# Kernel tuning notes

Measured on AMD Instinct MI355X. Metric: run time of the kernel, lower is better.

The kernel has to match this reference:

```python
import jax, jax.numpy as jnp
import numpy as np

SCALE = 2
K = 5          # up_kernel
GROUPS = 1     # up_group
COMP = 64      # compressed_channels


def _conv2d(x, w, b, padding):
    out = jax.lax.conv_general_dilated(
        x, w, window_strides=(1, 1),
        padding=[(padding, padding), (padding, padding)],
        dimension_numbers=('NCHW', 'OIHW', 'NCHW'))
    return out + b[None, :, None, None]


def _pixel_shuffle(x, r):
    b, crr, h, w = x.shape
    c = crr // (r * r)
    x = x.reshape(b, c, r, r, h, w)
    x = x.transpose(0, 1, 4, 2, 5, 3)  # b, c, h, r, w, r
    return x.reshape(b, c, h * r, w * r)


def setup_inputs() -> dict:
    key = jax.random.key(0)
    k1, k2, k3 = jax.random.split(key, 3)
    C = 256
    x = jax.random.normal(k1, (4, C, 128, 128), dtype=jnp.float32)
    mask_ch = SCALE * SCALE * K * K * GROUPS  # 100
    W1 = jax.random.normal(k2, (COMP, C, 1, 1), dtype=jnp.float32) * 0.05
    b1 = jnp.zeros((COMP,), dtype=jnp.float32)
    W2 = jax.random.normal(k3, (mask_ch, COMP, 3, 3), dtype=jnp.float32) * 0.05
    b2 = jnp.zeros((mask_ch,), dtype=jnp.float32)
    return {'x': x, 'W1': W1, 'b1': b1, 'W2': W2, 'b2': b2}


def reference(x, W1, b1, W2, b2):
    b, c, h, w = x.shape
    s, k, g = SCALE, K, GROUPS
    H, W = h * s, w * s
    # channel compressor (1x1) + mask encoder (3x3, pad 1)
    feat = _conv2d(x, W1, b1, 0)
    mask = _conv2d(feat, W2, b2, 1)            # (b, s^2*k^2*g, h, w)
    mask = _pixel_shuffle(mask, s)             # (b, k^2*g, H, W)
    mask = mask.reshape(b, g, k * k, H, W)
    mask = jax.nn.softmax(mask, axis=2)
    # nearest upsample
    x_up = jnp.repeat(jnp.repeat(x, s, axis=2), s, axis=3)  # (b, c, H, W)
    pad = k // 2
    xp = jnp.pad(x_up, ((0, 0), (0, 0), (pad, pad), (pad, pad)))
    xg = xp.reshape(b, g, c // g, H + 2 * pad, W + 2 * pad)
    # fused gather-multiply-reduce over the k*k window (avoids the huge unfold tensor)
    out = jnp.zeros((b, g, c // g, H, W), x.dtype)
    for i in range(k):
        for j in range(k):
            out = out + xg[:, :, :, i:i + H, j:j + W] * mask[:, :, None, i * k + j]
    return out.reshape(b, c, H, W)
```

## Files before the change

kernel.cpp:

```cpp
#include <hip/hip_runtime.h>

#define HW 16384
#define CIN 256
#define NCOMP 64
#define MASKC 100
#define NB 4
#define COPAD 112
#define KSTEPS 18

typedef __attribute__((ext_vector_type(8))) short bf16x8;
typedef __attribute__((ext_vector_type(4))) float f32x4;
typedef __attribute__((ext_vector_type(4), aligned(4))) float f4u;

__device__ inline ushort f2bf(float f) {
  uint x = __float_as_uint(f);
  return (ushort)((x + 0x7fffu + ((x >> 16) & 1u)) >> 16);
}

__device__ __forceinline__ void softmax_agg(const float* ldsM, int px, int rr,
                                            int h, float* wr9) {
  #pragma unroll
  for (int i = 0; i < 9; i++) wr9[i] = 0.f;

  float m[25], mx = -1e30f;
  #pragma unroll
  for (int kk = 0; kk < 25; kk++) {
    m[kk] = ldsM[(kk * 2 + (rr & 1)) * 129 + px];
    mx = fmaxf(mx, m[kk]);
  }
  float s = 0.f;
  #pragma unroll
  for (int kk = 0; kk < 25; kk++) { m[kk] = __expf(m[kk] - mx); s += m[kk]; }
  float inv = 1.f / s;
  const int r1 = rr >> 1, r2 = rr & 1;
  #pragma unroll
  for (int i = 0; i < 5; i++)
    #pragma unroll
    for (int j = 0; j < 5; j++) {
      const int dy = (r1 + i - 2) >> 1;
      const int dx = (r2 + j - 2) >> 1;
      wr9[(dy + 1) * 3 + (dx + 1)] += m[i * 5 + j] * inv;
    }

  #pragma unroll
  for (int dy = -1; dy <= 1; dy++) {
    bool vy = (unsigned)(h + dy) < 128u;
    #pragma unroll
    for (int dx = -1; dx <= 1; dx++) {
      bool vx = (unsigned)(px + dx) < 128u;
      if (!(vy && vx)) wr9[(dy + 1) * 3 + dx + 1] = 0.f;
    }
  }
}

__global__ __launch_bounds__(512) void conv1x1_mfma(const float* __restrict__ x,
    const ushort* __restrict__ W1b, const float* __restrict__ b1,
    ushort* __restrict__ feat_t) {
  int tid = threadIdx.x, bid = blockIdx.x;
  int b = bid >> 7, h = bid & 127;
  int wave = tid >> 6, lane = tid & 63;
  int l15 = lane & 15, l4 = lane >> 4;

  const float* xb = x + ((size_t)b << 22) + h * 128;
  int n = wave * 16 + l15;

  f32x4 acc[4];
  #pragma unroll
  for (int mt = 0; mt < 4; mt++) acc[mt] = (f32x4){0.f, 0.f, 0.f, 0.f};

  #pragma unroll
  for (int s = 0; s < 8; s++) {
    int k0 = s * 32 + l4 * 8;
    union { bf16x8 v; ushort us[8]; } bf;
    #pragma unroll
    for (int j = 0; j < 8; j++)
      bf.us[j] = f2bf(xb[((size_t)(k0 + j) << 14) + n]);
    #pragma unroll
    for (int mt = 0; mt < 4; mt++) {
      bf16x8 af = *(const bf16x8*)(W1b + (((mt * 8 + s) << 6) + lane) * 8);
      acc[mt] = __builtin_amdgcn_mfma_f32_16x16x32_bf16(af, bf.v, acc[mt], 0, 0, 0);
    }
  }

  ushort* fb = feat_t + (((size_t)(b << 14) + h * 128 + n) << 6);
  #pragma unroll
  for (int mt = 0; mt < 4; mt++) {
    float4 bv = *(const float4*)(b1 + mt * 16 + l4 * 4);
    const float* bvp = (const float*)&bv;
    uint u0 = (uint)f2bf(acc[mt][0] + bvp[0]) | ((uint)f2bf(acc[mt][1] + bvp[1]) << 16);
    uint u1 = (uint)f2bf(acc[mt][2] + bvp[2]) | ((uint)f2bf(acc[mt][3] + bvp[3]) << 16);
    uint2 st; st.x = u0; st.y = u1;
    *(uint2*)(fb + mt * 16 + l4 * 4) = st;
  }
}

__global__ __launch_bounds__(256) void wprep_k(const float* __restrict__ W2,
    const float* __restrict__ W1, ushort* __restrict__ Wr,
    ushort* __restrict__ W1b) {
  int i = blockIdx.x * 256 + threadIdx.x;
  if (i < 64512) {
    int e = i & 7, lane = (i >> 3) & 63, sm = i >> 9;
    int s = sm % 18, mt = sm / 18;
    int l15 = lane & 15, l4 = lane >> 4;
    int co = mt * 16 + l15;
    int ci = (s & 1) * 32 + l4 * 8 + e;
    int k = s >> 1;
    float v = (co < MASKC) ? W2[(co * 64 + ci) * 9 + k] : 0.f;
    Wr[i] = f2bf(v);
  } else if (i < 64512 + 16384) {
    int j = i - 64512;
    int e = j & 7, lane = (j >> 3) & 63, sm = j >> 9;
    int s = sm & 7, mt = sm >> 3;
    int l15 = lane & 15, l4 = lane >> 4;
    int co = mt * 16 + l15;
    int ci = s * 32 + l4 * 8 + e;
    W1b[j] = f2bf(W1[co * 256 + ci]);
  }
}

__global__ __launch_bounds__(512, 4) void conv3x3_combine(const ushort* __restrict__ feat_t,
    const ushort* __restrict__ Wr, const float* __restrict__ b2,
    const float* __restrict__ x, float* __restrict__ out) {
  __shared__ __align__(16) char smem[50 * 129 * 4 + 64];
  int tid = threadIdx.x;
  int wid = (blockIdx.x & 7) * 64 + (blockIdx.x >> 3);
  int b = wid >> 7, h = wid & 127;
  int wave = tid >> 6, lane = tid & 63;
  int l15 = lane & 15, l4 = lane >> 4;

  f32x4 acc[7];
  #pragma unroll
  for (int mt = 0; mt < 7; mt++) acc[mt] = (f32x4){0.f, 0.f, 0.f, 0.f};

  int cb = wave * 16;
  const ushort* fb = feat_t + (((size_t)b << 14) << 6);

  #pragma unroll
  for (int s = 0; s < KSTEPS; s++) {
    const int k = s >> 1;
    const int r = k / 3;
    const int dx = k % 3 - 1;
    const int ci0 = (s & 1) * 32;

    int hh = h - 1 + r;
    int gc = cb + l15 + dx;
    bf16x8 bfrag = {0, 0, 0, 0, 0, 0, 0, 0};
    if ((unsigned)hh < 128u && (unsigned)gc < 128u)
      bfrag = *(const bf16x8*)(fb + (((size_t)(hh * 128 + gc)) << 6) + ci0 + l4 * 8);

    #pragma unroll
    for (int mt = 0; mt < 7; mt++) {
      bf16x8 afrag = *(const bf16x8*)(Wr + (((mt * 18 + s) << 6) + lane) * 8);
      acc[mt] = __builtin_amdgcn_mfma_f32_16x16x32_bf16(afrag, bfrag, acc[mt], 0, 0, 0);
    }
  }

  float* ldsM = (float*)smem;
  float wr9[9];
  int px = tid & 127, rr = tid >> 7;

  #pragma unroll
  for (int mt = 0; mt < 7; mt++) {
    int kkd = mt * 4 + l4;
    if (kkd < 25) {
      int co0 = mt * 16 + l4 * 4;
      ldsM[(kkd * 2 + 0) * 129 + cb + l15] = acc[mt][0] + b2[co0 + 0];
      ldsM[(kkd * 2 + 1) * 129 + cb + l15] = acc[mt][1] + b2[co0 + 1];
    }
  }
  __syncthreads();

  if (rr < 2) softmax_agg(ldsM, px, rr, h, wr9);
  __syncthreads();

  #pragma unroll
  for (int mt = 0; mt < 7; mt++) {
    int kkd = mt * 4 + l4;
    if (kkd < 25) {
      int co0 = mt * 16 + l4 * 4;
      ldsM[(kkd * 2 + 0) * 129 + cb + l15] = acc[mt][2] + b2[co0 + 2];
      ldsM[(kkd * 2 + 1) * 129 + cb + l15] = acc[mt][3] + b2[co0 + 3];
    }
  }
  __syncthreads();

  if (rr >= 2) softmax_agg(ldsM, px, rr, h, wr9);
  __syncthreads();

  float* wlds = (float*)smem;
  {
    #pragma unroll
    for (int i = 0; i < 9; i++) wlds[px * 37 + rr * 9 + i] = wr9[i];
  }
  __syncthreads();

  {
    int pp = tid & 63, g = tid >> 6;
    int w0 = pp * 2;
    float wcA[36], wcB[36];
    #pragma unroll
    for (int i = 0; i < 36; i++) wcA[i] = wlds[w0 * 37 + i];
    #pragma unroll
    for (int i = 0; i < 36; i++) wcB[i] = wlds[(w0 + 1) * 37 + i];

    int cc0 = w0 - 1;
    cc0 = (cc0 < 0) ? 0 : ((cc0 > 124) ? 124 : cc0);
    int off = w0 - 1 - cc0;
    bool o0 = (off == 0), om = (off < 0);

    int ys[3] = {max(h - 1, 0) * 128, h * 128, min(h + 1, 127) * 128};
    const float* xbase = x + ((size_t)b << 22) + cc0;
    float* ob = out + (((size_t)b * CIN) << 16) + ((2 * h) << 8) + 4 * pp;

    #pragma unroll 2
    for (int cc = 0; cc < 32; cc++) {
      int c = cc * 8 + g;
      const float* xc = xbase + ((size_t)c << 14);
      float a0 = 0.f, a1 = 0.f, a2 = 0.f, a3 = 0.f;
      float b0 = 0.f, b1v = 0.f, b2v = 0.f, b3 = 0.f;
      #pragma unroll
      for (int dy = 0; dy < 3; dy++) {
        f4u f = *(const f4u*)(xc + ys[dy]);
        float vA0 = o0 ? f[0] : (om ? 0.f  : f[1]);
        float vA1 = o0 ? f[1] : (om ? f[0] : f[2]);
        float vA2 = o0 ? f[2] : (om ? f[1] : f[3]);
        float vB2 = o0 ? f[3] : (om ? f[2] : 0.f);
        a0 += wcA[0*9+dy*3+0]*vA0 + wcA[0*9+dy*3+1]*vA1 + wcA[0*9+dy*3+2]*vA2;
        a1 += wcA[1*9+dy*3+0]*vA0 + wcA[1*9+dy*3+1]*vA1 + wcA[1*9+dy*3+2]*vA2;
        a2 += wcA[2*9+dy*3+0]*vA0 + wcA[2*9+dy*3+1]*vA1 + wcA[2*9+dy*3+2]*vA2;
        a3 += wcA[3*9+dy*3+0]*vA0 + wcA[3*9+dy*3+1]*vA1 + wcA[3*9+dy*3+2]*vA2;
        b0  += wcB[0*9+dy*3+0]*vA1 + wcB[0*9+dy*3+1]*vA2 + wcB[0*9+dy*3+2]*vB2;
        b1v += wcB[1*9+dy*3+0]*vA1 + wcB[1*9+dy*3+1]*vA2 + wcB[1*9+dy*3+2]*vB2;
        b2v += wcB[2*9+dy*3+0]*vA1 + wcB[2*9+dy*3+1]*vA2 + wcB[2*9+dy*3+2]*vB2;
        b3  += wcB[3*9+dy*3+0]*vA1 + wcB[3*9+dy*3+1]*vA2 + wcB[3*9+dy*3+2]*vB2;
      }
      float* oc = ob + ((size_t)c << 16);
      float4 o0v; o0v.x = a0; o0v.y = a1; o0v.z = b0;  o0v.w = b1v;
      float4 o1v; o1v.x = a2; o1v.y = a3; o1v.z = b2v; o1v.w = b3;
      *(float4*)(oc) = o0v;
      *(float4*)(oc + 256) = o1v;
    }
  }
}

extern "C" void kernel_launch(void* const* d_in, const int* in_sizes, int n_in,
                              void* d_out, int out_size, void* d_ws, size_t ws_size,
                              hipStream_t stream) {
  const float* x  = (const float*)d_in[0];
  const float* W1 = (const float*)d_in[1];
  const float* b1 = (const float*)d_in[2];
  const float* W2 = (const float*)d_in[3];
  const float* b2 = (const float*)d_in[4];
  float* out  = (float*)d_out;

  char* ws = (char*)d_ws;
  ushort* feat_t = (ushort*)ws;
  ushort* Wr     = (ushort*)(ws + 8388608);
  ushort* W1b    = (ushort*)(ws + 8388608 + 129024);

  wprep_k<<<316, 256, 0, stream>>>(W2, W1, Wr, W1b);
  conv1x1_mfma<<<NB * 128, 512, 0, stream>>>(x, W1b, b1, feat_t);
  conv3x3_combine<<<NB * 128, 512, 0, stream>>>(feat_t, Wr, b2, x, out);
}
```

Baseline: 108.1 us.

## Split fused conv3x3+combine into mask kernel and separate wider-grid combine kernel

Splits the fused conv3x3/softmax/combine kernel in two. The first kernel writes the aggregated 3x3 mask weights (36 floats per pixel) to a workspace buffer. A new combine kernel then reads them with a 2D grid that spreads channels over four blocks per row. The goal is more parallelism and occupancy for the bandwidth-bound combine stage, which no longer shares the register and LDS footprint of the MFMA phase. The cost is one extra launch and a global write/read of about 9 MB of weights.

```diff
diff --git a/kernel.cpp b/kernel.cpp
--- a/kernel.cpp
+++ b/kernel.cpp
@@ -118,9 +118,9 @@
   }
 }
 
-__global__ __launch_bounds__(512, 4) void conv3x3_combine(const ushort* __restrict__ feat_t,
+__global__ __launch_bounds__(512, 4) void conv3x3_mask(const ushort* __restrict__ feat_t,
     const ushort* __restrict__ Wr, const float* __restrict__ b2,
-    const float* __restrict__ x, float* __restrict__ out) {
+    float* __restrict__ wagg) {
   __shared__ __align__(16) char smem[50 * 129 * 4 + 64];
   int tid = threadIdx.x;
   int wid = (blockIdx.x & 7) * 64 + (blockIdx.x >> 3);
@@ -195,51 +195,77 @@
   __syncthreads();
 
   {
-    int pp = tid & 63, g = tid >> 6;
-    int w0 = pp * 2;
-    float wcA[36], wcB[36];
-    #pragma unroll
-    for (int i = 0; i < 36; i++) wcA[i] = wlds[w0 * 37 + i];
-    #pragma unroll
-    for (int i = 0; i < 36; i++) wcB[i] = wlds[(w0 + 1) * 37 + i];
-
-    int cc0 = w0 - 1;
-    cc0 = (cc0 < 0) ? 0 : ((cc0 > 124) ? 124 : cc0);
-    int off = w0 - 1 - cc0;
-    bool o0 = (off == 0), om = (off < 0);
-
-    int ys[3] = {max(h - 1, 0) * 128, h * 128, min(h + 1, 127) * 128};
-    const float* xbase = x + ((size_t)b << 22) + cc0;
-    float* ob = out + (((size_t)b * CIN) << 16) + ((2 * h) << 8) + 4 * pp;
-
-    #pragma unroll 2
-    for (int cc = 0; cc < 32; cc++) {
-      int c = cc * 8 + g;
-      const float* xc = xbase + ((size_t)c << 14);
-      float a0 = 0.f, a1 = 0.f, a2 = 0.f, a3 = 0.f;
-      float b0 = 0.f, b1v = 0.f, b2v = 0.f, b3 = 0.f;
-      #pragma unroll
-      for (int dy = 0; dy < 3; dy++) {
-        f4u f = *(const f4u*)(xc + ys[dy]);
-        float vA0 = o0 ? f[0] : (om ? 0.f  : f[1]);
-        float vA1 = o0 ? f[1] : (om ? f[0] : f[2]);
-        float vA2 = o0 ? f[2] : (om ? f[1] : f[3]);
-        float vB2 = o0 ? f[3] : (om ? f[2] : 0.f);
-        a0 += wcA[0*9+dy*3+0]*vA0 + wcA[0*9+dy*3+1]*vA1 + wcA[0*9+dy*3+2]*vA2;
-        a1 += wcA[1*9+dy*3+0]*vA0 + wcA[1*9+dy*3+1]*vA1 + wcA[1*9+dy*3+2]*vA2;
-        a2 += wcA[2*9+dy*3+0]*vA0 + wcA[2*9+dy*3+1]*vA1 + wcA[2*9+dy*3+2]*vA2;
-        a3 += wcA[3*9+dy*3+0]*vA0 + wcA[3*9+dy*3+1]*vA1 + wcA[3*9+dy*3+2]*vA2;
-        b0  += wcB[0*9+dy*3+0]*vA1 + wcB[0*9+dy*3+1]*vA2 + wcB[0*9+dy*3+2]*vB2;
-        b1v += wcB[1*9+dy*3+0]*vA1 + wcB[1*9+dy*3+1]*vA2 + wcB[1*9+dy*3+2]*vB2;
-        b2v += wcB[2*9+dy*3+0]*vA1 + wcB[2*9+dy*3+1]*vA2 + wcB[2*9+dy*3+2]*vB2;
-        b3  += wcB[3*9+dy*3+0]*vA1 + wcB[3*9+dy*3+1]*vA2 + wcB[3*9+dy*3+2]*vB2;
-      }
-      float* oc = ob + ((size_t)c << 16);
-      float4 o0v; o0v.x = a0; o0v.y = a1; o0v.z = b0;  o0v.w = b1v;
-      float4 o1v; o1v.x = a2; o1v.y = a3; o1v.z = b2v; o1v.w = b3;
-      *(float4*)(oc) = o0v;
-      *(float4*)(oc + 256) = o1v;
-    }
+    float* wrow = wagg + ((size_t)(b << 14) + h * 128) * 36;
+    #pragma unroll
+    for (int it = 0; it < 9; it++) {
+      int j = tid + it * 512;
+      int p = j / 36, e = j - p * 36;
+      wrow[j] = wlds[p * 37 + e];
+    }
+  }
+}
+
+__global__ __launch_bounds__(256) void combine_k(const float* __restrict__ x,
+    const float* __restrict__ wagg, float* __restrict__ out) {
+  int tid = threadIdx.x;
+  int wid = (blockIdx.x & 7) * 64 + (blockIdx.x >> 3);
+  int b = wid >> 7, h = wid & 127;
+  int pp = tid & 63, sg = tid >> 6;
+  int c0 = blockIdx.y * 64 + sg * 16;
+  int w0 = pp * 2;
+
+  float wcA[36], wcB[36];
+  {
+    const float4* wv = (const float4*)(wagg + ((size_t)(b << 14) + h * 128 + w0) * 36);
+    #pragma unroll
+    for (int q = 0; q < 9; q++) {
+      float4 v = wv[q];
+      wcA[q * 4 + 0] = v.x; wcA[q * 4 + 1] = v.y;
+      wcA[q * 4 + 2] = v.z; wcA[q * 4 + 3] = v.w;
+    }
+    #pragma unroll
+    for (int q = 0; q < 9; q++) {
+      float4 v = wv[9 + q];
+      wcB[q * 4 + 0] = v.x; wcB[q * 4 + 1] = v.y;
+      wcB[q * 4 + 2] = v.z; wcB[q * 4 + 3] = v.w;
+    }
+  }
+
+  int cc0 = w0 - 1;
+  cc0 = (cc0 < 0) ? 0 : ((cc0 > 124) ? 124 : cc0);
+  int off = w0 - 1 - cc0;
+  bool o0 = (off == 0), om = (off < 0);
+
+  int ys[3] = {max(h - 1, 0) * 128, h * 128, min(h + 1, 127) * 128};
+  const float* xbase = x + ((size_t)b << 22) + cc0 + (((size_t)c0) << 14);
+  float* ob = out + (((size_t)(b * CIN + c0)) << 16) + ((2 * h) << 8) + 4 * pp;
+
+  #pragma unroll 2
+  for (int cc = 0; cc < 16; cc++) {
+    const float* xc = xbase + ((size_t)cc << 14);
+    float a0 = 0.f, a1 = 0.f, a2 = 0.f, a3 = 0.f;
+    float b0 = 0.f, b1v = 0.f, b2v = 0.f, b3 = 0.f;
+    #pragma unroll
+    for (int dy = 0; dy < 3; dy++) {
+      f4u f = *(const f4u*)(xc + ys[dy]);
+      float vA0 = o0 ? f[0] : (om ? 0.f  : f[1]);
+      float vA1 = o0 ? f[1] : (om ? f[0] : f[2]);
+      float vA2 = o0 ? f[2] : (om ? f[1] : f[3]);
+      float vB2 = o0 ? f[3] : (om ? f[2] : 0.f);
+      a0 += wcA[0*9+dy*3+0]*vA0 + wcA[0*9+dy*3+1]*vA1 + wcA[0*9+dy*3+2]*vA2;
+      a1 += wcA[1*9+dy*3+0]*vA0 + wcA[1*9+dy*3+1]*vA1 + wcA[1*9+dy*3+2]*vA2;
+      a2 += wcA[2*9+dy*3+0]*vA0 + wcA[2*9+dy*3+1]*vA1 + wcA[2*9+dy*3+2]*vA2;
+      a3 += wcA[3*9+dy*3+0]*vA0 + wcA[3*9+dy*3+1]*vA1 + wcA[3*9+dy*3+2]*vA2;
+      b0  += wcB[0*9+dy*3+0]*vA1 + wcB[0*9+dy*3+1]*vA2 + wcB[0*9+dy*3+2]*vB2;
+      b1v += wcB[1*9+dy*3+0]*vA1 + wcB[1*9+dy*3+1]*vA2 + wcB[1*9+dy*3+2]*vB2;
+      b2v += wcB[2*9+dy*3+0]*vA1 + wcB[2*9+dy*3+1]*vA2 + wcB[2*9+dy*3+2]*vB2;
+      b3  += wcB[3*9+dy*3+0]*vA1 + wcB[3*9+dy*3+1]*vA2 + wcB[3*9+dy*3+2]*vB2;
+    }
+    float* oc = ob + ((size_t)cc << 16);
+    float4 o0v; o0v.x = a0; o0v.y = a1; o0v.z = b0;  o0v.w = b1v;
+    float4 o1v; o1v.x = a2; o1v.y = a3; o1v.z = b2v; o1v.w = b3;
+    *(float4*)(oc) = o0v;
+    *(float4*)(oc + 256) = o1v;
   }
 }
 
@@ -257,8 +283,10 @@
   ushort* feat_t = (ushort*)ws;
   ushort* Wr     = (ushort*)(ws + 8388608);
   ushort* W1b    = (ushort*)(ws + 8388608 + 129024);
+  float*  wagg   = (float*)(ws + 8388608 + 129024 + 32768);
 
   wprep_k<<<316, 256, 0, stream>>>(W2, W1, Wr, W1b);
   conv1x1_mfma<<<NB * 128, 512, 0, stream>>>(x, W1b, b1, feat_t);
-  conv3x3_combine<<<NB * 128, 512, 0, stream>>>(feat_t, Wr, b2, x, out);
-}
+  conv3x3_mask<<<NB * 128, 512, 0, stream>>>(feat_t, Wr, b2, wagg);
+  combine_k<<<dim3(NB * 128, 4), 256, 0, stream>>>(x, wagg, out);
+}
```

New measurement: 113.9 us. +5.4%, slower.

## Fuse 1x1 compressor conv into 3x3 mask kernel via LDS halo tile

Applied to the files above, without the earlier changes.

Removes the separate 1x1 conv kernel and its global bf16 feature buffer. Each block now computes the compressed features for its three input rows (with halo) into a swizzled, zero-padded LDS tile, then runs the 3x3 MFMA conv from LDS. This drops a kernel launch and the feature write/read round trip. The cost is computing each row's 1x1 conv three times (once per neighbouring block), roughly tripling compressor reads of x and its MFMA work.

```diff
diff --git a/kernel.cpp b/kernel.cpp
--- a/kernel.cpp
+++ b/kernel.cpp
@@ -50,47 +50,6 @@
       bool vx = (unsigned)(px + dx) < 128u;
       if (!(vy && vx)) wr9[(dy + 1) * 3 + dx + 1] = 0.f;
     }
-  }
-}
-
-__global__ __launch_bounds__(512) void conv1x1_mfma(const float* __restrict__ x,
-    const ushort* __restrict__ W1b, const float* __restrict__ b1,
-    ushort* __restrict__ feat_t) {
-  int tid = threadIdx.x, bid = blockIdx.x;
-  int b = bid >> 7, h = bid & 127;
-  int wave = tid >> 6, lane = tid & 63;
-  int l15 = lane & 15, l4 = lane >> 4;
-
-  const float* xb = x + ((size_t)b << 22) + h * 128;
-  int n = wave * 16 + l15;
-
-  f32x4 acc[4];
-  #pragma unroll
-  for (int mt = 0; mt < 4; mt++) acc[mt] = (f32x4){0.f, 0.f, 0.f, 0.f};
-
-  #pragma unroll
-  for (int s = 0; s < 8; s++) {
-    int k0 = s * 32 + l4 * 8;
-    union { bf16x8 v; ushort us[8]; } bf;
-    #pragma unroll
-    for (int j = 0; j < 8; j++)
-      bf.us[j] = f2bf(xb[((size_t)(k0 + j) << 14) + n]);
-    #pragma unroll
-    for (int mt = 0; mt < 4; mt++) {
-      bf16x8 af = *(const bf16x8*)(W1b + (((mt * 8 + s) << 6) + lane) * 8);
-      acc[mt] = __builtin_amdgcn_mfma_f32_16x16x32_bf16(af, bf.v, acc[mt], 0, 0, 0);
-    }
-  }
-
-  ushort* fb = feat_t + (((size_t)(b << 14) + h * 128 + n) << 6);
-  #pragma unroll
-  for (int mt = 0; mt < 4; mt++) {
-    float4 bv = *(const float4*)(b1 + mt * 16 + l4 * 4);
-    const float* bvp = (const float*)&bv;
-    uint u0 = (uint)f2bf(acc[mt][0] + bvp[0]) | ((uint)f2bf(acc[mt][1] + bvp[1]) << 16);
-    uint u1 = (uint)f2bf(acc[mt][2] + bvp[2]) | ((uint)f2bf(acc[mt][3] + bvp[3]) << 16);
-    uint2 st; st.x = u0; st.y = u1;
-    *(uint2*)(fb + mt * 16 + l4 * 4) = st;
   }
 }
 
@@ -118,35 +77,82 @@
   }
 }
 
-__global__ __launch_bounds__(512, 4) void conv3x3_combine(const ushort* __restrict__ feat_t,
+__global__ __launch_bounds__(512, 4) void carafe_fused(const float* __restrict__ x,
+    const ushort* __restrict__ W1b, const float* __restrict__ b1,
     const ushort* __restrict__ Wr, const float* __restrict__ b2,
-    const float* __restrict__ x, float* __restrict__ out) {
-  __shared__ __align__(16) char smem[50 * 129 * 4 + 64];
+    float* __restrict__ out) {
+  __shared__ __align__(16) char smem[49920];
   int tid = threadIdx.x;
   int wid = (blockIdx.x & 7) * 64 + (blockIdx.x >> 3);
   int b = wid >> 7, h = wid & 127;
   int wave = tid >> 6, lane = tid & 63;
   int l15 = lane & 15, l4 = lane >> 4;
 
+  {
+    uint4 z = {0, 0, 0, 0};
+    for (int i = tid; i < 3120; i += 512)
+      *(uint4*)(smem + i * 16) = z;
+  }
+  __syncthreads();
+
+  const float* xbase = x + ((size_t)b << 22);
+  #pragma unroll
+  for (int tt = 0; tt < 3; tt++) {
+    int t = wave * 3 + tt;
+    int r = t >> 3, px0 = (t & 7) << 4;
+    int hh = h - 1 + r;
+    if (hh >= 0 && hh < 128) {
+      const float* xw = xbase + hh * 128 + px0 + l15;
+      f32x4 a4[4];
+      #pragma unroll
+      for (int mt = 0; mt < 4; mt++) a4[mt] = (f32x4){0.f, 0.f, 0.f, 0.f};
+      #pragma unroll
+      for (int s = 0; s < 8; s++) {
+        int k0 = s * 32 + l4 * 8;
+        union { bf16x8 v; ushort us[8]; } bf;
+        #pragma unroll
+        for (int j = 0; j < 8; j++)
+          bf.us[j] = f2bf(xw[(size_t)(k0 + j) << 14]);
+        #pragma unroll
+        for (int mt = 0; mt < 4; mt++) {
+          bf16x8 af = *(const bf16x8*)(W1b + (((mt * 8 + s) << 6) + lane) * 8);
+          a4[mt] = __builtin_amdgcn_mfma_f32_16x16x32_bf16(af, bf.v, a4[mt], 0, 0, 0);
+        }
+      }
+      int col = px0 + l15 + 1;
+      uint cr = (uint)((r * 130 + col) << 7);
+      uint swz = (uint)((col & 7) << 4);
+      #pragma unroll
+      for (int mt = 0; mt < 4; mt++) {
+        int co0 = mt * 16 + l4 * 4;
+        float4 bv = *(const float4*)(b1 + co0);
+        const float* bvp = (const float*)&bv;
+        uint u0 = (uint)f2bf(a4[mt][0] + bvp[0]) | ((uint)f2bf(a4[mt][1] + bvp[1]) << 16);
+        uint u1 = (uint)f2bf(a4[mt][2] + bvp[2]) | ((uint)f2bf(a4[mt][3] + bvp[3]) << 16);
+        uint2 st; st.x = u0; st.y = u1;
+        *(uint2*)(smem + ((cr + co0 * 2) ^ swz)) = st;
+      }
+    }
+  }
+  __syncthreads();
+
   f32x4 acc[7];
   #pragma unroll
   for (int mt = 0; mt < 7; mt++) acc[mt] = (f32x4){0.f, 0.f, 0.f, 0.f};
 
   int cb = wave * 16;
-  const ushort* fb = feat_t + (((size_t)b << 14) << 6);
 
   #pragma unroll
   for (int s = 0; s < KSTEPS; s++) {
     const int k = s >> 1;
     const int r = k / 3;
-    const int dx = k % 3 - 1;
+    const int dxi = k % 3;
     const int ci0 = (s & 1) * 32;
 
-    int hh = h - 1 + r;
-    int gc = cb + l15 + dx;
-    bf16x8 bfrag = {0, 0, 0, 0, 0, 0, 0, 0};
-    if ((unsigned)hh < 128u && (unsigned)gc < 128u)
-      bfrag = *(const bf16x8*)(fb + (((size_t)(hh * 128 + gc)) << 6) + ci0 + l4 * 8);
+    int col = cb + l15 + dxi;
+    uint addr = (uint)(((r * 130 + col) << 7) + ci0 * 2 + l4 * 16)
+              ^ (uint)((col & 7) << 4);
+    bf16x8 bfrag = *(const bf16x8*)(smem + addr);
 
     #pragma unroll
     for (int mt = 0; mt < 7; mt++) {
@@ -154,6 +160,7 @@
       acc[mt] = __builtin_amdgcn_mfma_f32_16x16x32_bf16(afrag, bfrag, acc[mt], 0, 0, 0);
     }
   }
+  __syncthreads();
 
   float* ldsM = (float*)smem;
   float wr9[9];
@@ -209,13 +216,13 @@
     bool o0 = (off == 0), om = (off < 0);
 
     int ys[3] = {max(h - 1, 0) * 128, h * 128, min(h + 1, 127) * 128};
-    const float* xbase = x + ((size_t)b << 22) + cc0;
+    const float* xw = xbase + cc0;
     float* ob = out + (((size_t)b * CIN) << 16) + ((2 * h) << 8) + 4 * pp;
 
     #pragma unroll 2
     for (int cc = 0; cc < 32; cc++) {
       int c = cc * 8 + g;
-      const float* xc = xbase + ((size_t)c << 14);
+      const float* xc = xw + ((size_t)c << 14);
       float a0 = 0.f, a1 = 0.f, a2 = 0.f, a3 = 0.f;
       float b0 = 0.f, b1v = 0.f, b2v = 0.f, b3 = 0.f;
       #pragma unroll
@@ -254,11 +261,9 @@
   float* out  = (float*)d_out;
 
   char* ws = (char*)d_ws;
-  ushort* feat_t = (ushort*)ws;
-  ushort* Wr     = (ushort*)(ws + 8388608);
-  ushort* W1b    = (ushort*)(ws + 8388608 + 129024);
+  ushort* Wr  = (ushort*)ws;
+  ushort* W1b = (ushort*)(ws + 129024);
 
   wprep_k<<<316, 256, 0, stream>>>(W2, W1, Wr, W1b);
-  conv1x1_mfma<<<NB * 128, 512, 0, stream>>>(x, W1b, b1, feat_t);
-  conv3x3_combine<<<NB * 128, 512, 0, stream>>>(feat_t, Wr, b2, x, out);
-}
+  carafe_fused<<<NB * 128, 512, 0, stream>>>(x, W1b, b1, Wr, b2, out);
+}
```

Result: slower. 112.8 us (+4.4%).

## Software-pipeline x loads in combine loop and transpose weight LDS layout

Applied to the files above, without the earlier changes.

The final combine loop now double-buffers the three x row loads per channel, prefetching the next channel's rows while computing the current one, so global-load latency is hidden. The per-pixel weight staging in LDS changes from pixel-major with stride 37 to weight-index-major with stride 130, which changes the bank access pattern of the weight reads. The extra prefetch registers may raise register pressure under the 512-thread, 4-block launch bound.

```diff
diff --git a/kernel.cpp b/kernel.cpp
--- a/kernel.cpp
+++ b/kernel.cpp
@@ -5,7 +5,6 @@
 #define NCOMP 64
 #define MASKC 100
 #define NB 4
-#define COPAD 112
 #define KSTEPS 18
 
 typedef __attribute__((ext_vector_type(8))) short bf16x8;
@@ -190,7 +189,7 @@
   float* wlds = (float*)smem;
   {
     #pragma unroll
-    for (int i = 0; i < 9; i++) wlds[px * 37 + rr * 9 + i] = wr9[i];
+    for (int i = 0; i < 9; i++) wlds[(rr * 9 + i) * 130 + px] = wr9[i];
   }
   __syncthreads();
 
@@ -199,9 +198,9 @@
     int w0 = pp * 2;
     float wcA[36], wcB[36];
     #pragma unroll
-    for (int i = 0; i < 36; i++) wcA[i] = wlds[w0 * 37 + i];
-    #pragma unroll
-    for (int i = 0; i < 36; i++) wcB[i] = wlds[(w0 + 1) * 37 + i];
+    for (int i = 0; i < 36; i++) wcA[i] = wlds[i * 130 + w0];
+    #pragma unroll
+    for (int i = 0; i < 36; i++) wcB[i] = wlds[i * 130 + w0 + 1];
 
     int cc0 = w0 - 1;
     cc0 = (cc0 < 0) ? 0 : ((cc0 > 124) ? 124 : cc0);
@@ -209,37 +208,55 @@
     bool o0 = (off == 0), om = (off < 0);
 
     int ys[3] = {max(h - 1, 0) * 128, h * 128, min(h + 1, 127) * 128};
-    const float* xbase = x + ((size_t)b << 22) + cc0;
+    const float* xw = x + ((size_t)b << 22) + cc0;
     float* ob = out + (((size_t)b * CIN) << 16) + ((2 * h) << 8) + 4 * pp;
 
-    #pragma unroll 2
-    for (int cc = 0; cc < 32; cc++) {
-      int c = cc * 8 + g;
-      const float* xc = xbase + ((size_t)c << 14);
-      float a0 = 0.f, a1 = 0.f, a2 = 0.f, a3 = 0.f;
-      float b0 = 0.f, b1v = 0.f, b2v = 0.f, b3 = 0.f;
+#define CS(F, CIDX) do {                                                      \
+    float a0 = 0.f, a1 = 0.f, a2 = 0.f, a3 = 0.f;                             \
+    float b0 = 0.f, b1v = 0.f, b2v = 0.f, b3 = 0.f;                           \
+    _Pragma("unroll")                                                         \
+    for (int dy = 0; dy < 3; dy++) {                                          \
+      f4u f = (F)[dy];                                                        \
+      float vA0 = o0 ? f[0] : (om ? 0.f  : f[1]);                             \
+      float vA1 = o0 ? f[1] : (om ? f[0] : f[2]);                             \
+      float vA2 = o0 ? f[2] : (om ? f[1] : f[3]);                             \
+      float vB2 = o0 ? f[3] : (om ? f[2] : 0.f);                              \
+      a0 += wcA[0*9+dy*3+0]*vA0 + wcA[0*9+dy*3+1]*vA1 + wcA[0*9+dy*3+2]*vA2;  \
+      a1 += wcA[1*9+dy*3+0]*vA0 + wcA[1*9+dy*3+1]*vA1 + wcA[1*9+dy*3+2]*vA2;  \
+      a2 += wcA[2*9+dy*3+0]*vA0 + wcA[2*9+dy*3+1]*vA1 + wcA[2*9+dy*3+2]*vA2;  \
+      a3 += wcA[3*9+dy*3+0]*vA0 + wcA[3*9+dy*3+1]*vA1 + wcA[3*9+dy*3+2]*vA2;  \
+      b0  += wcB[0*9+dy*3+0]*vA1 + wcB[0*9+dy*3+1]*vA2 + wcB[0*9+dy*3+2]*vB2; \
+      b1v += wcB[1*9+dy*3+0]*vA1 + wcB[1*9+dy*3+1]*vA2 + wcB[1*9+dy*3+2]*vB2; \
+      b2v += wcB[2*9+dy*3+0]*vA1 + wcB[2*9+dy*3+1]*vA2 + wcB[2*9+dy*3+2]*vB2; \
+      b3  += wcB[3*9+dy*3+0]*vA1 + wcB[3*9+dy*3+1]*vA2 + wcB[3*9+dy*3+2]*vB2; \
+    }                                                                         \
+    float* oc = ob + ((size_t)(CIDX) << 16);                                  \
+    float4 o0v; o0v.x = a0; o0v.y = a1; o0v.z = b0;  o0v.w = b1v;             \
+    float4 o1v; o1v.x = a2; o1v.y = a3; o1v.z = b2v; o1v.w = b3;              \
+    *(float4*)(oc) = o0v;                                                     \
+    *(float4*)(oc + 256) = o1v;                                               \
+  } while (0)
+
+    f4u fA[3], fB[3];
+    {
+      const float* xc = xw + ((size_t)g << 14);
       #pragma unroll
-      for (int dy = 0; dy < 3; dy++) {
-        f4u f = *(const f4u*)(xc + ys[dy]);
-        float vA0 = o0 ? f[0] : (om ? 0.f  : f[1]);
-        float vA1 = o0 ? f[1] : (om ? f[0] : f[2]);
-        float vA2 = o0 ? f[2] : (om ? f[1] : f[3]);
-        float vB2 = o0 ? f[3] : (om ? f[2] : 0.f);
-        a0 += wcA[0*9+dy*3+0]*vA0 + wcA[0*9+dy*3+1]*vA1 + wcA[0*9+dy*3+2]*vA2;
-        a1 += wcA[1*9+dy*3+0]*vA0 + wcA[1*9+dy*3+1]*vA1 + wcA[1*9+dy*3+2]*vA2;
-        a2 += wcA[2*9+dy*3+0]*vA0 + wcA[2*9+dy*3+1]*vA1 + wcA[2*9+dy*3+2]*vA2;
-        a3 += wcA[3*9+dy*3+0]*vA0 + wcA[3*9+dy*3+1]*vA1 + wcA[3*9+dy*3+2]*vA2;
-        b0  += wcB[0*9+dy*3+0]*vA1 + wcB[0*9+dy*3+1]*vA2 + wcB[0*9+dy*3+2]*vB2;
-        b1v += wcB[1*9+dy*3+0]*vA1 + wcB[1*9+dy*3+1]*vA2 + wcB[1*9+dy*3+2]*vB2;
-        b2v += wcB[2*9+dy*3+0]*vA1 + wcB[2*9+dy*3+1]*vA2 + wcB[2*9+dy*3+2]*vB2;
-        b3  += wcB[3*9+dy*3+0]*vA1 + wcB[3*9+dy*3+1]*vA2 + wcB[3*9+dy*3+2]*vB2;
+      for (int dy = 0; dy < 3; dy++) fA[dy] = *(const f4u*)(xc + ys[dy]);
+    }
+    #pragma unroll 1
+    for (int cc = 0; cc < 32; cc += 2) {
+      const float* xcB = xw + ((size_t)((cc + 1) * 8 + g) << 14);
+      #pragma unroll
+      for (int dy = 0; dy < 3; dy++) fB[dy] = *(const f4u*)(xcB + ys[dy]);
+      CS(fA, cc * 8 + g);
+      if (cc + 2 < 32) {
+        const float* xcA = xw + ((size_t)((cc + 2) * 8 + g) << 14);
+        #pragma unroll
+        for (int dy = 0; dy < 3; dy++) fA[dy] = *(const f4u*)(xcA + ys[dy]);
       }
-      float* oc = ob + ((size_t)c << 16);
-      float4 o0v; o0v.x = a0; o0v.y = a1; o0v.z = b0;  o0v.w = b1v;
-      float4 o1v; o1v.x = a2; o1v.y = a3; o1v.z = b2v; o1v.w = b3;
-      *(float4*)(oc) = o0v;
-      *(float4*)(oc + 256) = o1v;
-    }
+      CS(fB, (cc + 1) * 8 + g);
+    }
+#undef CS
   }
 }
 
```

Result: slower. 126.7 us (+17.2%).
